# Kernel optimization log

Measured on AMD Instinct MI355X. Metric: run time of the kernel, lower is better.

## Reference

```python
import jax, jax.numpy as jnp
import numpy as np

MARGIN = 0.2
EPS = 1e-6  # torch.pairwise_distance adds eps to the difference before the norm


def setup_inputs() -> dict:
    key = jax.random.key(0)
    k1, k2, k3 = jax.random.split(key, 3)
    B, D = 8192, 128
    emb1 = jax.random.normal(k1, (B, D), dtype=jnp.float32)
    emb2 = jax.random.normal(k2, (B, D), dtype=jnp.float32)
    target = jax.random.randint(k3, (B,), 0, 2, dtype=jnp.int64)
    return {"emb1": emb1, "emb2": emb2, "target": target}


def reference(emb1, emb2, target):
    B, D = emb1.shape
    # torch.pairwise_distance(a, b) = ||a - b + EPS||_2; expand the square:
    # |a-b+eps|^2 = |a|^2 + |b|^2 - 2 a.b + 2*eps*(sum(a)-sum(b)) + D*eps^2
    sq = (
        jnp.sum(emb1 * emb1, axis=-1)[:, None]
        + jnp.sum(emb2 * emb2, axis=-1)[None, :]
        - 2.0 * (emb1 @ emb2.T)
        + 2.0 * EPS * (jnp.sum(emb1, axis=-1)[:, None] - jnp.sum(emb2, axis=-1)[None, :])
        + D * EPS * EPS
    )
    dist = jnp.sqrt(jnp.maximum(sq, 0.0))  # [B, B]: dist[i, j] = ||emb1[i] - emb2[j] + eps||

    pos = target == 1
    neg = target == 0
    # hardest positive: max over columns j with target[j]==1; hardest negative: min over target[j]==0
    pos_max = jnp.max(jnp.where(pos[None, :], dist, -jnp.inf), axis=1)  # [B]
    neg_min = jnp.min(jnp.where(neg[None, :], dist, jnp.inf), axis=1)   # [B]
    per_anchor = jnp.maximum(pos_max - neg_min + MARGIN, 0.0)
    anchor_w = pos.astype(dist.dtype)
    # mean over anchors (rows i with target[i]==1)
    return jnp.sum(per_anchor * anchor_w) / jnp.sum(anchor_w)
```

## Files before the change

kernel.cpp:

```cpp
#include <hip/hip_runtime.h>
#include <hip/hip_bf16.h>
#include <math.h>


#define DDIM   128
#define SPLITS 8
#define MARGIN 0.2f
#define EPS    1e-6f
#define SENT   1e30f

#define PANEL_BYTES  16384
#define CPCN_BYTES   (2048 * 4)

typedef unsigned short ushort_t;
typedef __attribute__((ext_vector_type(8))) short short8;
typedef __attribute__((ext_vector_type(4))) float f32x4;
typedef __attribute__((ext_vector_type(4))) unsigned short ushort4_t;

__device__ __forceinline__ ushort_t f2bf(float f) {
    unsigned int u = __float_as_uint(f);
    u = (u + 0x7FFFu + ((u >> 16) & 1u)) >> 16;
    return (ushort_t)u;
}

__device__ __forceinline__ void g2lds16(const void* g, void* lds) {
    __builtin_amdgcn_global_load_lds(
        (const __attribute__((address_space(1))) unsigned int*)g,
        (__attribute__((address_space(3))) unsigned int*)lds,
        16, 0, 0);
}

__global__ void prep_kernel(const float* __restrict__ e1, const float* __restrict__ e2,
                            const int* __restrict__ target,
                            ushort_t* __restrict__ e1b, ushort_t* __restrict__ e2b,
                            float* __restrict__ rowterm,
                            float* __restrict__ cpos, float* __restrict__ cneg,
                            float* __restrict__ redsum, int* __restrict__ ticket, int B) {
    if (blockIdx.x == 0) {
        if (threadIdx.x == 0) { redsum[0] = 0.f; redsum[1] = 0.f; }
        else if (threadIdx.x == 1) *ticket = 0;
    }
    int gr  = blockIdx.x * 32 + (threadIdx.x >> 3);
    int seg = threadIdx.x & 7;
    bool first = gr < B;
    int r = first ? gr : gr - B;
    const float* src = (first ? e1 : e2) + (size_t)r * DDIM;
    ushort_t*    dst = (first ? e1b : e2b) + (size_t)r * DDIM;
    const float sc = first ? -2.f : 1.f;
    float s = 0.f, n = 0.f;
    #pragma unroll
    for (int it = 0; it < 4; ++it) {
        int e0 = (seg + it * 8) * 4;
        float4 v = *(const float4*)(src + e0);
        ushort4_t o;
        o.x = f2bf(sc * v.x); o.y = f2bf(sc * v.y);
        o.z = f2bf(sc * v.z); o.w = f2bf(sc * v.w);
        *(ushort4_t*)(dst + e0) = o;
        s += v.x + v.y + v.z + v.w;
        n += v.x * v.x + v.y * v.y + v.z * v.z + v.w * v.w;
    }
    #pragma unroll
    for (int m = 1; m <= 4; m <<= 1) {
        s += __shfl_xor(s, m, 64);
        n += __shfl_xor(n, m, 64);
    }
    if (seg == 0) {
        if (first) {
            rowterm[r] = n + 2.f * EPS * s + (float)DDIM * EPS * EPS;
        } else {
            float ct = n - 2.f * EPS * s;
            int tg = target[r];
            cpos[r] = (tg == 1) ? ct : -SENT;
            cneg[r] = (tg == 0) ? ct :  SENT;
        }
    }
}

__device__ __forceinline__ void stage_panel(const ushort_t* __restrict__ pcol,
                                            unsigned char* __restrict__ lds,
                                            int w, int l) {
    const ushort_t* g = pcol + (size_t)(w * 16 + (l & 15)) * DDIM + (l >> 4) * 8;
    unsigned char* lp = lds + w * 4096;
    #pragma unroll
    for (int it = 0; it < 4; ++it)
        g2lds16(g + it * 32, lp + it * 1024);
}

__global__ __launch_bounds__(256, 3)
void tile_kernel(const ushort_t* __restrict__ e1b, const ushort_t* __restrict__ e2b,
                 const float* __restrict__ cpos, const float* __restrict__ cneg,
                 float* __restrict__ pmp, float* __restrict__ nmp, int B) {
    __shared__ __align__(16) unsigned char smRaw[2 * PANEL_BYTES + CPCN_BYTES];
    unsigned char* Bs0  = smRaw;
    unsigned char* Bs1  = smRaw + PANEL_BYTES;
    float*         smCp = (float*)(smRaw + 2 * PANEL_BYTES);
    float*         smCn = smCp + 1024;

    const int tid = threadIdx.x;
    const int w   = tid >> 6;
    const int l   = tid & 63;
    const int lq  = l >> 4;
    const int lm  = l & 15;
    const int row0 = blockIdx.x * 128;
    const int col0 = blockIdx.y * 1024;
    const int nPanels = 16;

    const int wr = (w >> 1) * 64;
    const int wc = (w & 1) * 32;
    const int jj0 = (w & 1) * 2;

    stage_panel(e2b + (size_t)col0 * DDIM, Bs0, w, l);
    g2lds16(cpos + col0 + w * 256 + l * 4, smCp + w * 256);
    g2lds16(cneg + col0 + w * 256 + l * 4, smCn + w * 256);

    const ushort_t* aG = e1b + (size_t)(row0 + wr + lm) * DDIM + lq * 8;
    short8 afr[4][4];
    #pragma unroll
    for (int i = 0; i < 4; ++i)
        #pragma unroll
        for (int k4 = 0; k4 < 4; ++k4)
            afr[i][k4] = *(const short8*)(aG + i * 16 * DDIM + k4 * 32);

    const unsigned char* bLane = Bs0 + (size_t)l * 16;

    float pm[4][4], nm[4][4];
    #pragma unroll
    for (int i = 0; i < 4; ++i)
        #pragma unroll
        for (int r = 0; r < 4; ++r) { pm[i][r] = -SENT; nm[i][r] = SENT; }

    __syncthreads();

    for (int p = 0; p < nPanels; ++p) {
        if (p) __builtin_amdgcn_s_barrier();

        if (p + 1 < nPanels) {
            stage_panel(e2b + (size_t)(col0 + (p + 1) * 64) * DDIM,
                        (p & 1) ? Bs0 : Bs1, w, l);
            asm volatile("s_waitcnt vmcnt(4)" ::: "memory");
        } else {
            asm volatile("s_waitcnt vmcnt(0)" ::: "memory");
        }
        __builtin_amdgcn_s_barrier();

        const unsigned char* bl = bLane + (p & 1) * PANEL_BYTES;

        f32x4 accA[4], accB[4];
        #pragma unroll
        for (int i = 0; i < 4; ++i) {
            accA[i] = (f32x4){0.f, 0.f, 0.f, 0.f};
            accB[i] = (f32x4){0.f, 0.f, 0.f, 0.f};
        }

        #pragma unroll
        for (int k4 = 0; k4 < 4; ++k4) {
            const short8 b0 = *(const short8*)(bl + ((jj0 + 0) * 4 + k4) * 1024);
            const short8 b1 = *(const short8*)(bl + ((jj0 + 1) * 4 + k4) * 1024);
            #pragma unroll
            for (int i = 0; i < 4; ++i)
                accA[i] = __builtin_amdgcn_mfma_f32_16x16x32_bf16(
                              afr[i][k4], b0, accA[i], 0, 0, 0);
            #pragma unroll
            for (int i = 0; i < 4; ++i)
                accB[i] = __builtin_amdgcn_mfma_f32_16x16x32_bf16(
                              afr[i][k4], b1, accB[i], 0, 0, 0);
        }

        {
            const int lcb = p * 64 + wc + lm;
            const float cp0 = smCp[lcb],      cn0 = smCn[lcb];
            const float cp1 = smCp[lcb + 16], cn1 = smCn[lcb + 16];
            #pragma unroll
            for (int i = 0; i < 4; ++i)
                #pragma unroll
                for (int r = 0; r < 4; ++r) {
                    const float d0 = accA[i][r];
                    const float d1 = accB[i][r];
                    pm[i][r] = fmaxf(fmaxf(pm[i][r], d0 + cp0), d1 + cp1);
                    nm[i][r] = fminf(fminf(nm[i][r], d0 + cn0), d1 + cn1);
                }
        }
    }

    #pragma unroll
    for (int m = 1; m < 16; m <<= 1) {
        #pragma unroll
        for (int i = 0; i < 4; ++i)
            #pragma unroll
            for (int r = 0; r < 4; ++r) {
                pm[i][r] = fmaxf(pm[i][r], __shfl_xor(pm[i][r], m, 64));
                nm[i][r] = fminf(nm[i][r], __shfl_xor(nm[i][r], m, 64));
            }
    }

    float* smP = (float*)smRaw;
    float* smN = smP + 128;
    if ((w & 1) == 1 && lm == 0) {
        #pragma unroll
        for (int i = 0; i < 4; ++i)
            #pragma unroll
            for (int r = 0; r < 4; ++r) {
                int lr = wr + i * 16 + lq * 4 + r;
                smP[lr] = pm[i][r];
                smN[lr] = nm[i][r];
            }
    }
    __syncthreads();
    if ((w & 1) == 0 && lm == 0) {
        #pragma unroll
        for (int i = 0; i < 4; ++i)
            #pragma unroll
            for (int r = 0; r < 4; ++r) {
                int lr = wr + i * 16 + lq * 4 + r;
                smP[lr] = fmaxf(pm[i][r], smP[lr]);
                smN[lr] = fminf(nm[i][r], smN[lr]);
            }
    }
    __syncthreads();
    if (tid < 128) {
        pmp[(size_t)blockIdx.y * B + row0 + tid] = smP[tid];
        nmp[(size_t)blockIdx.y * B + row0 + tid] = smN[tid];
    }
}

__global__ void reduce_kernel(const float* __restrict__ pmp, const float* __restrict__ nmp,
                              const float* __restrict__ rowterm, const int* __restrict__ target,
                              float* __restrict__ redsum, int* __restrict__ ticket,
                              float* __restrict__ out, int B) {
    int row = blockIdx.x * blockDim.x + threadIdx.x;
    float s = 0.f, c = 0.f;
    {
        float pmv = -SENT, nmv = SENT;
        #pragma unroll
        for (int sp = 0; sp < SPLITS; ++sp) {
            pmv = fmaxf(pmv, pmp[(size_t)sp * B + row]);
            nmv = fminf(nmv, nmp[(size_t)sp * B + row]);
        }
        float rt = rowterm[row];
        float dp = sqrtf(fmaxf(rt + pmv, 0.f));
        float dn = sqrtf(fmaxf(rt + nmv, 0.f));
        if (target[row] == 1) {
            s = fmaxf(dp - dn + MARGIN, 0.f);
            c = 1.f;
        }
    }
    #pragma unroll
    for (int off = 32; off > 0; off >>= 1) {
        s += __shfl_down(s, off, 64);
        c += __shfl_down(c, off, 64);
    }
    __shared__ float ls[4], lc[4];
    int wv = threadIdx.x >> 6, ln = threadIdx.x & 63;
    if (ln == 0) { ls[wv] = s; lc[wv] = c; }
    __syncthreads();
    if (threadIdx.x == 0) {
        float ss = ls[0] + ls[1] + ls[2] + ls[3];
        float cc = lc[0] + lc[1] + lc[2] + lc[3];
        atomicAdd(&redsum[0], ss);
        atomicAdd(&redsum[1], cc);
        __threadfence();
        int done = atomicAdd(ticket, 1);
        if (done == (int)gridDim.x - 1) {
            __threadfence();
            float fs = __hip_atomic_load(&redsum[0], __ATOMIC_RELAXED, __HIP_MEMORY_SCOPE_AGENT);
            float fc = __hip_atomic_load(&redsum[1], __ATOMIC_RELAXED, __HIP_MEMORY_SCOPE_AGENT);
            out[0] = fs / fc;
        }
    }
}

extern "C" void kernel_launch(void* const* d_in, const int* in_sizes, int n_in,
                              void* d_out, int out_size, void* d_ws, size_t ws_size,
                              hipStream_t stream) {
    const float* e1     = (const float*)d_in[0];
    const float* e2     = (const float*)d_in[1];
    const int*   target = (const int*)d_in[2];
    float* out = (float*)d_out;
    const int B = in_sizes[2];

    char* p = (char*)d_ws;
    ushort_t* e1b  = (ushort_t*)p;   p += (size_t)B * DDIM * 2;
    ushort_t* e2b  = (ushort_t*)p;   p += (size_t)B * DDIM * 2;
    float* rowterm = (float*)p;      p += (size_t)B * 4;
    float* cpos    = (float*)p;      p += (size_t)B * 4;
    float* cneg    = (float*)p;      p += (size_t)B * 4;
    float* pmp     = (float*)p;      p += (size_t)SPLITS * B * 4;
    float* nmp     = (float*)p;      p += (size_t)SPLITS * B * 4;
    float* redsum  = (float*)p;      p += 2 * 4;
    int*   ticket  = (int*)p;

    {
        int blocks = (2 * B) / 32;
        prep_kernel<<<blocks, 256, 0, stream>>>(e1, e2, target, e1b, e2b,
                                                rowterm, cpos, cneg,
                                                redsum, ticket, B);
    }
    {
        dim3 grid(B / 128, SPLITS);
        tile_kernel<<<grid, 256, 0, stream>>>(e1b, e2b, cpos, cneg, pmp, nmp, B);
    }
    reduce_kernel<<<32, 256, 0, stream>>>(pmp, nmp, rowterm, target,
                                          redsum, ticket, out, B);
}
```

Baseline: 91.52 us.

## Give each wave private LDS panel halves and drop per-panel block barriers

Each wave now stages only the 32 columns of each B panel it consumes into its own double-buffered LDS region. This replaces the shared 64-column panel staged by all four waves. Because no wave reads data another wave loaded, the two workgroup barriers per panel iteration are removed and each wave synchronises only on its own vmcnt. The cost is duplicated global/L2 loads: waves sharing a column half each fetch it, so B traffic per block doubles. LDS per block rises to 72KB and launch bounds drop from 3 to 2 blocks per CU, lowering occupancy.

```diff
diff --git a/kernel.cpp b/kernel.cpp
--- a/kernel.cpp
+++ b/kernel.cpp
@@ -9,7 +9,8 @@
 #define EPS    1e-6f
 #define SENT   1e30f
 
-#define PANEL_BYTES  16384
+#define HALF_BYTES   8192
+#define WAVE_LDS     (2 * HALF_BYTES)
 #define CPCN_BYTES   (2048 * 4)
 
 typedef unsigned short ushort_t;
@@ -76,25 +77,24 @@
     }
 }
 
-__device__ __forceinline__ void stage_panel(const ushort_t* __restrict__ pcol,
-                                            unsigned char* __restrict__ lds,
-                                            int w, int l) {
-    const ushort_t* g = pcol + (size_t)(w * 16 + (l & 15)) * DDIM + (l >> 4) * 8;
-    unsigned char* lp = lds + w * 4096;
-    #pragma unroll
-    for (int it = 0; it < 4; ++it)
-        g2lds16(g + it * 32, lp + it * 1024);
-}
-
-__global__ __launch_bounds__(256, 3)
+__device__ __forceinline__ void stage_half(const ushort_t* __restrict__ pcol,
+                                           unsigned char* __restrict__ lds,
+                                           int jj0, int l) {
+    const ushort_t* g = pcol + (size_t)(jj0 * 16 + (l & 15)) * DDIM + (l >> 4) * 8;
+    #pragma unroll
+    for (int c = 0; c < 8; ++c) {
+        const int jjrel = c >> 2, k4 = c & 3;
+        g2lds16(g + jjrel * 16 * DDIM + k4 * 32, lds + c * 1024);
+    }
+}
+
+__global__ __launch_bounds__(256, 2)
 void tile_kernel(const ushort_t* __restrict__ e1b, const ushort_t* __restrict__ e2b,
                  const float* __restrict__ cpos, const float* __restrict__ cneg,
                  float* __restrict__ pmp, float* __restrict__ nmp, int B) {
-    __shared__ __align__(16) unsigned char smRaw[2 * PANEL_BYTES + CPCN_BYTES];
-    unsigned char* Bs0  = smRaw;
-    unsigned char* Bs1  = smRaw + PANEL_BYTES;
-    float*         smCp = (float*)(smRaw + 2 * PANEL_BYTES);
-    float*         smCn = smCp + 1024;
+    __shared__ __align__(16) unsigned char smRaw[4 * WAVE_LDS + CPCN_BYTES];
+    float* smCp = (float*)(smRaw + 4 * WAVE_LDS);
+    float* smCn = smCp + 1024;
 
     const int tid = threadIdx.x;
     const int w   = tid >> 6;
@@ -105,13 +105,17 @@
     const int col0 = blockIdx.y * 1024;
     const int nPanels = 16;
 
-    const int wr = (w >> 1) * 64;
-    const int wc = (w & 1) * 32;
+    const int wr  = (w >> 1) * 64;
+    const int wc  = (w & 1) * 32;
     const int jj0 = (w & 1) * 2;
 
-    stage_panel(e2b + (size_t)col0 * DDIM, Bs0, w, l);
+    unsigned char* myLds = smRaw + w * WAVE_LDS;
+
     g2lds16(cpos + col0 + w * 256 + l * 4, smCp + w * 256);
     g2lds16(cneg + col0 + w * 256 + l * 4, smCn + w * 256);
+    stage_half(e2b + (size_t)col0 * DDIM, myLds, jj0, l);
+    asm volatile("s_waitcnt vmcnt(8)" ::: "memory");
+    __syncthreads();
 
     const ushort_t* aG = e1b + (size_t)(row0 + wr + lm) * DDIM + lq * 8;
     short8 afr[4][4];
@@ -121,7 +125,7 @@
         for (int k4 = 0; k4 < 4; ++k4)
             afr[i][k4] = *(const short8*)(aG + i * 16 * DDIM + k4 * 32);
 
-    const unsigned char* bLane = Bs0 + (size_t)l * 16;
+    const unsigned char* bLane = myLds + (size_t)l * 16;
 
     float pm[4][4], nm[4][4];
     #pragma unroll
@@ -129,21 +133,16 @@
         #pragma unroll
         for (int r = 0; r < 4; ++r) { pm[i][r] = -SENT; nm[i][r] = SENT; }
 
-    __syncthreads();
-
     for (int p = 0; p < nPanels; ++p) {
-        if (p) __builtin_amdgcn_s_barrier();
-
         if (p + 1 < nPanels) {
-            stage_panel(e2b + (size_t)(col0 + (p + 1) * 64) * DDIM,
-                        (p & 1) ? Bs0 : Bs1, w, l);
-            asm volatile("s_waitcnt vmcnt(4)" ::: "memory");
+            stage_half(e2b + (size_t)(col0 + (p + 1) * 64) * DDIM,
+                       myLds + ((p + 1) & 1) * HALF_BYTES, jj0, l);
+            asm volatile("s_waitcnt vmcnt(8)" ::: "memory");
         } else {
             asm volatile("s_waitcnt vmcnt(0)" ::: "memory");
         }
-        __builtin_amdgcn_s_barrier();
-
-        const unsigned char* bl = bLane + (p & 1) * PANEL_BYTES;
+
+        const unsigned char* bl = bLane + (p & 1) * HALF_BYTES;
 
         f32x4 accA[4], accB[4];
         #pragma unroll
@@ -154,8 +153,8 @@
 
         #pragma unroll
         for (int k4 = 0; k4 < 4; ++k4) {
-            const short8 b0 = *(const short8*)(bl + ((jj0 + 0) * 4 + k4) * 1024);
-            const short8 b1 = *(const short8*)(bl + ((jj0 + 1) * 4 + k4) * 1024);
+            const short8 b0 = *(const short8*)(bl + k4 * 1024);
+            const short8 b1 = *(const short8*)(bl + (4 + k4) * 1024);
             #pragma unroll
             for (int i = 0; i < 4; ++i)
                 accA[i] = __builtin_amdgcn_mfma_f32_16x16x32_bf16(
@@ -195,6 +194,7 @@
 
     float* smP = (float*)smRaw;
     float* smN = smP + 128;
+    __syncthreads();
     if ((w & 1) == 1 && lm == 0) {
         #pragma unroll
         for (int i = 0; i < 4; ++i)
```

Result: slower. 103.7 us (+13.3%).
